# Optimization experiments

Measured on AMD Instinct MI355X. Metric: run time of the kernel, lower is better.

## Reference

```python
import jax, jax.numpy as jnp
import numpy as np

INPUT_DIM, LATENT_DIM, NUM_HEADS, LATENT_RANK = 2048, 1024, 16, 256
HEAD_DIM = LATENT_DIM // NUM_HEADS


def _linear_params(key, in_dim, out_dim):
    kw, kb = jax.random.split(key)
    bound = 1.0 / np.sqrt(in_dim)
    W = jax.random.uniform(kw, (in_dim, out_dim), jnp.float32, -bound, bound)
    b = jax.random.uniform(kb, (out_dim,), jnp.float32, -bound, bound)
    return W, b


def setup_inputs() -> dict:
    key = jax.random.key(0)
    ks = jax.random.split(key, 7)
    latent = jax.random.normal(ks[0], (2, 1024, LATENT_DIM), jnp.float32)
    x = jax.random.normal(ks[1], (2, 4096, INPUT_DIM), jnp.float32)
    Wq, bq = _linear_params(ks[2], LATENT_DIM, LATENT_DIM)
    Wc, bc = _linear_params(ks[3], INPUT_DIM, LATENT_RANK)
    Wk, bk = _linear_params(ks[4], LATENT_RANK, LATENT_DIM)
    Wv, bv = _linear_params(ks[5], LATENT_RANK, LATENT_DIM)
    Wo, bo = _linear_params(ks[6], LATENT_DIM, LATENT_DIM)
    return {"latent": latent, "x": x,
            "Wq": Wq, "bq": bq, "Wc": Wc, "bc": bc,
            "Wk": Wk, "bk": bk, "Wv": Wv, "bv": bv,
            "Wo": Wo, "bo": bo}


def reference(latent, x, Wq, bq, Wc, bc, Wk, bk, Wv, bv, Wo, bo):
    B, L, _ = latent.shape
    S = x.shape[1]
    H, D = NUM_HEADS, HEAD_DIM
    Q = (latent @ Wq + bq).reshape(B, L, H, D).transpose(0, 2, 1, 3)   # (B,H,L,D)
    compressed = x @ Wc + bc                                            # (B,S,R)
    K = (compressed @ Wk + bk).reshape(B, S, H, D).transpose(0, 2, 1, 3)  # (B,H,S,D)
    V = (compressed @ Wv + bv).reshape(B, S, H, D).transpose(0, 2, 1, 3)  # (B,H,S,D)
    scores = jnp.einsum('bhld,bhsd->bhls', Q, K) / np.sqrt(D).astype(jnp.float32)
    attn_weights = jax.nn.softmax(scores, axis=-1)                      # (B,H,L,S)
    attn_out = jnp.einsum('bhls,bhsd->bhld', attn_weights, V)           # (B,H,L,D)
    attn_out = attn_out.transpose(0, 2, 1, 3).reshape(B, L, H * D)
    output = attn_out @ Wo + bo                                         # (B,L,latent_dim)
    return output, attn_weights
```

## Files before the change

### kernel.cpp

```cpp
#include <hip/hip_runtime.h>

typedef short sv8 __attribute__((ext_vector_type(8)));
typedef float fv4 __attribute__((ext_vector_type(4)));

#define MFMA16(a, b, c) __builtin_amdgcn_mfma_f32_16x16x32_bf16((a), (b), (c), 0, 0, 0)

__device__ __forceinline__ unsigned short f2bf(float f) {
    unsigned u = __builtin_bit_cast(unsigned, f);
    unsigned r = (u + 0x7FFF + ((u >> 16) & 1)) >> 16;
    return (unsigned short)r;
}

constexpr int BB = 2, LL = 1024, SS = 4096, LD = 1024, HH = 16, DD = 64;

constexpr size_t NX = (size_t)2 * 4096 * 2048;
constexpr size_t NL = (size_t)2 * 1024 * 1024;

__global__ __launch_bounds__(256) void convert_inputs(
    const float* __restrict__ x, const float* __restrict__ latent,
    unsigned short* __restrict__ xb, unsigned short* __restrict__ lb)
{
    size_t i = ((size_t)blockIdx.x * 256 + threadIdx.x) * 8;
    const float* src; unsigned short* dst;
    if (i < NX) { src = x + i; dst = xb + i; }
    else        { size_t j = i - NX; src = latent + j; dst = lb + j; }
    float4 a = *(const float4*)src;
    float4 b = *(const float4*)(src + 4);
    ushort4 o0 = {f2bf(a.x), f2bf(a.y), f2bf(a.z), f2bf(a.w)};
    ushort4 o1 = {f2bf(b.x), f2bf(b.y), f2bf(b.z), f2bf(b.w)};
    *(ushort4*)dst = o0;
    *(ushort4*)(dst + 4) = o1;
}

__global__ __launch_bounds__(256) void transpose_weights(
    const float* __restrict__ Wc, const float* __restrict__ Wk, const float* __restrict__ Wv,
    const float* __restrict__ Wq, const float* __restrict__ Wo,
    unsigned short* __restrict__ Tc, unsigned short* __restrict__ Tk,
    unsigned short* __restrict__ Tv, unsigned short* __restrict__ Tq,
    unsigned short* __restrict__ To)
{
    __shared__ __align__(16) unsigned short tile[64][68];
    int bid = blockIdx.x;
    const float* W; unsigned short* T; int K, N, tix;
    if (bid < 128)      { W = Wc; T = Tc; K = 2048; N = 256;  tix = bid; }
    else if (bid < 192) { W = Wk; T = Tk; K = 256;  N = 1024; tix = bid - 128; }
    else if (bid < 256) { W = Wv; T = Tv; K = 256;  N = 1024; tix = bid - 192; }
    else if (bid < 512) { W = Wq; T = Tq; K = 1024; N = 1024; tix = bid - 256; }
    else                { W = Wo; T = To; K = 1024; N = 1024; tix = bid - 512; }
    int tn = N >> 6;
    int k0 = (tix / tn) << 6, n0 = (tix % tn) << 6;
    int t = threadIdx.x;
    int r = t >> 4, c4 = (t & 15) * 4;
#pragma unroll
    for (int i = 0; i < 4; i++) {
        int k = r + i * 16;
        float4 f = *(const float4*)(W + (size_t)(k0 + k) * N + n0 + c4);
        tile[k][c4 + 0] = f2bf(f.x); tile[k][c4 + 1] = f2bf(f.y);
        tile[k][c4 + 2] = f2bf(f.z); tile[k][c4 + 3] = f2bf(f.w);
    }
    __syncthreads();
#pragma unroll
    for (int i = 0; i < 4; i++) {
        int n = r + i * 16;
        ushort4 o;
        o.x = tile[c4 + 0][n]; o.y = tile[c4 + 1][n];
        o.z = tile[c4 + 2][n]; o.w = tile[c4 + 3][n];
        *(ushort4*)(T + (size_t)(n0 + n) * K + k0 + c4) = o;
    }
}

__global__ __launch_bounds__(256) void transpose_v(
    const unsigned short* __restrict__ V, unsigned short* __restrict__ Vt)
{
    __shared__ __align__(16) unsigned short tile[64][68];
    int s0 = blockIdx.x * 64;
    int h = blockIdx.y, b = blockIdx.z;
    int t = threadIdx.x;
    int r = t >> 4, c4 = (t & 15) * 4;
#pragma unroll
    for (int i = 0; i < 4; i++) {
        int s = r + i * 16;
        ushort4 v = *(const ushort4*)(V + (size_t)(b * SS + s0 + s) * LD + h * DD + c4);
        tile[s][c4 + 0] = v.x; tile[s][c4 + 1] = v.y;
        tile[s][c4 + 2] = v.z; tile[s][c4 + 3] = v.w;
    }
    __syncthreads();
#pragma unroll
    for (int i = 0; i < 4; i++) {
        int d = r + i * 16;
        ushort4 o;
        o.x = tile[c4 + 0][d]; o.y = tile[c4 + 1][d];
        o.z = tile[c4 + 2][d]; o.w = tile[c4 + 3][d];
        *(ushort4*)(Vt + ((size_t)(b * HH + h) * DD + d) * SS + s0 + c4) = o;
    }
}

template<int BM, int BN, bool C_F32>
__global__ __launch_bounds__(256) void gemm_bias(
    const unsigned short* __restrict__ Ag, const unsigned short* __restrict__ Bt,
    const float* __restrict__ bias, void* __restrict__ Cg,
    int M, int N, int K, float scale)
{
    constexpr int LDT = 40;
    __shared__ __align__(16) unsigned short As[BM * LDT];
    __shared__ __align__(16) unsigned short Bs[BN * LDT];
    __shared__ float bias_s[BN];
    const int t = threadIdx.x;
    const int m0 = blockIdx.x * BM, n0 = blockIdx.y * BN;
    for (int i = t; i < BN; i += 256) bias_s[i] = bias[n0 + i];
    const int w = t >> 6, lane = t & 63, l15 = lane & 15, quad = lane >> 4;
    constexpr int WM = BM / 2, WN = BN / 2;
    constexpr int MT = WM / 16, NT = WN / 16;
    const int wm = (w >> 1) * WM, wn = (w & 1) * WN;
    fv4 acc[MT][NT] = {};
    const int r4 = t >> 2, c8 = (t & 3) * 8;
    constexpr int AI = BM / 64, BI = BN / 64;
    const unsigned short* Aptr = Ag + (size_t)(m0 + r4) * K + c8;
    const unsigned short* Bptr = Bt + (size_t)(n0 + r4) * K + c8;
    sv8 areg[AI], breg[BI];
#pragma unroll
    for (int i = 0; i < AI; i++) areg[i] = *(const sv8*)(Aptr + (size_t)(i * 64) * K);
#pragma unroll
    for (int i = 0; i < BI; i++) breg[i] = *(const sv8*)(Bptr + (size_t)(i * 64) * K);
    for (int k0 = 0; k0 < K; k0 += 32) {
#pragma unroll
        for (int i = 0; i < AI; i++) *(sv8*)&As[(r4 + i * 64) * LDT + c8] = areg[i];
#pragma unroll
        for (int i = 0; i < BI; i++) *(sv8*)&Bs[(r4 + i * 64) * LDT + c8] = breg[i];
        __syncthreads();
        if (k0 + 32 < K) {
#pragma unroll
            for (int i = 0; i < AI; i++)
                areg[i] = *(const sv8*)(Aptr + (size_t)(i * 64) * K + k0 + 32);
#pragma unroll
            for (int i = 0; i < BI; i++)
                breg[i] = *(const sv8*)(Bptr + (size_t)(i * 64) * K + k0 + 32);
        }
        sv8 af[MT], bfr[NT];
#pragma unroll
        for (int mt = 0; mt < MT; mt++)
            af[mt] = *(const sv8*)&As[(wm + mt * 16 + l15) * LDT + quad * 8];
#pragma unroll
        for (int nt = 0; nt < NT; nt++)
            bfr[nt] = *(const sv8*)&Bs[(wn + nt * 16 + l15) * LDT + quad * 8];
#pragma unroll
        for (int mt = 0; mt < MT; mt++)
#pragma unroll
            for (int nt = 0; nt < NT; nt++)
                acc[mt][nt] = MFMA16(af[mt], bfr[nt], acc[mt][nt]);
        __syncthreads();
    }
#pragma unroll
    for (int mt = 0; mt < MT; mt++) {
#pragma unroll
        for (int nt = 0; nt < NT; nt++) {
            int col = n0 + wn + nt * 16 + l15;
            float bb = bias_s[wn + nt * 16 + l15];
#pragma unroll
            for (int r = 0; r < 4; r++) {
                int row = m0 + wm + mt * 16 + quad * 4 + r;
                float vv = (acc[mt][nt][r] + bb) * scale;
                if constexpr (C_F32) ((float*)Cg)[(size_t)row * N + col] = vv;
                else ((unsigned short*)Cg)[(size_t)row * N + col] = f2bf(vv);
            }
        }
    }
}

constexpr int SC  = 128;
constexpr int KLD = 72;
constexpr int VLD = 136;

__global__ __launch_bounds__(256) void attn_kernel(
    const unsigned short* __restrict__ Qw,
    const unsigned short* __restrict__ Kw,
    const unsigned short* __restrict__ Vtw,
    float* __restrict__ Wout,
    unsigned short* __restrict__ Ow)
{
    __shared__ __align__(16) unsigned short Ks[SC * KLD];
    __shared__ __align__(16) unsigned short Vs[DD * VLD];
    __shared__ __align__(16) unsigned short Ps[4 * 16 * VLD];
    const int bid = blockIdx.x;
    const int lt = bid & 15, h = (bid >> 4) & 15, b = bid >> 8;
    const int l0 = lt * 64;
    const int t = threadIdx.x, w = t >> 6, lane = t & 63, l15 = lane & 15, quad = lane >> 4;

    const unsigned short* qrow = Qw + (size_t)(b * LL + l0 + w * 16 + l15) * LD + h * DD;
    const sv8 aq0 = *(const sv8*)(qrow + quad * 8);
    const sv8 aq1 = *(const sv8*)(qrow + 32 + quad * 8);

    const unsigned short* kg0 = Kw + (size_t)(b * SS) * LD + h * DD;
    const int kr = t >> 3, kc = (t & 7) * 8;

    float lsum[4] = {0.f, 0.f, 0.f, 0.f};
    sv8 kreg[4];
#pragma unroll
    for (int i = 0; i < 4; i++)
        kreg[i] = *(const sv8*)(kg0 + (size_t)(kr + i * 32) * LD + kc);
    for (int s0 = 0; s0 < SS; s0 += SC) {
#pragma unroll
        for (int i = 0; i < 4; i++)
            *(sv8*)&Ks[(kr + i * 32) * KLD + kc] = kreg[i];
        __syncthreads();
        if (s0 + SC < SS) {
            const unsigned short* kg = kg0 + (size_t)(s0 + SC) * LD;
#pragma unroll
            for (int i = 0; i < 4; i++)
                kreg[i] = *(const sv8*)(kg + (size_t)(kr + i * 32) * LD + kc);
        }
#pragma unroll
        for (int c = 0; c < 8; c++) {
            sv8 b0 = *(const sv8*)&Ks[(c * 16 + l15) * KLD + quad * 8];
            sv8 b1 = *(const sv8*)&Ks[(c * 16 + l15) * KLD + 32 + quad * 8];
            fv4 sc = {0.f, 0.f, 0.f, 0.f};
            __builtin_amdgcn_s_setprio(1);
            sc = MFMA16(aq0, b0, sc);
            sc = MFMA16(aq1, b1, sc);
            __builtin_amdgcn_s_setprio(0);
#pragma unroll
            for (int r = 0; r < 4; r++) lsum[r] += __expf(sc[r]);
        }
        __syncthreads();
    }
    float inv_l[4];
#pragma unroll
    for (int r = 0; r < 4; r++) {
        float v = lsum[r];
        v += __shfl_xor(v, 1); v += __shfl_xor(v, 2);
        v += __shfl_xor(v, 4); v += __shfl_xor(v, 8);
        inv_l[r] = 1.0f / v;
    }

    fv4 oacc[4] = {};
    float* wbase = Wout + ((size_t)((b * HH + h) * LL + l0 + w * 16)) * SS;
    const unsigned short* vg0 = Vtw + (size_t)(b * HH + h) * DD * SS;
    const int vd = t >> 4, vc = (t & 15) * 8;
    sv8 vreg[4];
#pragma unroll
    for (int i = 0; i < 4; i++)
        kreg[i] = *(const sv8*)(kg0 + (size_t)(kr + i * 32) * LD + kc);
#pragma unroll
    for (int i = 0; i < 4; i++)
        vreg[i] = *(const sv8*)(vg0 + (size_t)(vd + i * 16) * SS + vc);
    for (int s0 = 0; s0 < SS; s0 += SC) {
#pragma unroll
        for (int i = 0; i < 4; i++)
            *(sv8*)&Ks[(kr + i * 32) * KLD + kc] = kreg[i];
#pragma unroll
        for (int i = 0; i < 4; i++)
            *(sv8*)&Vs[(vd + i * 16) * VLD + vc] = vreg[i];
        __syncthreads();
        if (s0 + SC < SS) {
            const unsigned short* kg = kg0 + (size_t)(s0 + SC) * LD;
#pragma unroll
            for (int i = 0; i < 4; i++)
                kreg[i] = *(const sv8*)(kg + (size_t)(kr + i * 32) * LD + kc);
#pragma unroll
            for (int i = 0; i < 4; i++)
                vreg[i] = *(const sv8*)(vg0 + (size_t)(vd + i * 16) * SS + s0 + SC + vc);
        }
        float* wp0 = wbase + s0;
#pragma unroll
        for (int c = 0; c < 8; c++) {
            sv8 b0 = *(const sv8*)&Ks[(c * 16 + l15) * KLD + quad * 8];
            sv8 b1 = *(const sv8*)&Ks[(c * 16 + l15) * KLD + 32 + quad * 8];
            fv4 sc = {0.f, 0.f, 0.f, 0.f};
            __builtin_amdgcn_s_setprio(1);
            sc = MFMA16(aq0, b0, sc);
            sc = MFMA16(aq1, b1, sc);
            __builtin_amdgcn_s_setprio(0);
#pragma unroll
            for (int r = 0; r < 4; r++) {
                float wv = __expf(sc[r]) * inv_l[r];
                wp0[(size_t)(quad * 4 + r) * SS + c * 16 + l15] = wv;
                Ps[(w * 16 + quad * 4 + r) * VLD + c * 16 + l15] = f2bf(wv);
            }
        }
        sv8 ap[4];
#pragma unroll
        for (int ks = 0; ks < 4; ks++)
            ap[ks] = *(const sv8*)&Ps[(w * 16 + l15) * VLD + ks * 32 + quad * 8];
        __builtin_amdgcn_s_setprio(1);
#pragma unroll
        for (int dt = 0; dt < 4; dt++)
#pragma unroll
            for (int ks = 0; ks < 4; ks++) {
                sv8 bv = *(const sv8*)&Vs[(dt * 16 + l15) * VLD + ks * 32 + quad * 8];
                oacc[dt] = MFMA16(ap[ks], bv, oacc[dt]);
            }
        __builtin_amdgcn_s_setprio(0);
        __syncthreads();
    }
    unsigned short* obase = Ow + (size_t)(b * LL + l0 + w * 16) * LD + h * DD;
#pragma unroll
    for (int dt = 0; dt < 4; dt++)
#pragma unroll
        for (int r = 0; r < 4; r++)
            obase[(size_t)(quad * 4 + r) * LD + dt * 16 + l15] = f2bf(oacc[dt][r]);
}

extern "C" void kernel_launch(void* const* d_in, const int* in_sizes, int n_in,
                              void* d_out, int out_size, void* d_ws, size_t ws_size,
                              hipStream_t stream) {
    const float* latent = (const float*)d_in[0];
    const float* x      = (const float*)d_in[1];
    const float* Wq = (const float*)d_in[2];
    const float* bq = (const float*)d_in[3];
    const float* Wc = (const float*)d_in[4];
    const float* bc = (const float*)d_in[5];
    const float* Wk = (const float*)d_in[6];
    const float* bk = (const float*)d_in[7];
    const float* Wv = (const float*)d_in[8];
    const float* bv = (const float*)d_in[9];
    const float* Wo = (const float*)d_in[10];
    const float* bo = (const float*)d_in[11];

    float* out   = (float*)d_out;
    float* attnw = out + (size_t)2 * 1024 * 1024;

    char* ws = (char*)d_ws;
    size_t off = 0;
    auto alloc = [&](size_t bytes) -> void* {
        void* p = ws + off; off += (bytes + 255) & ~(size_t)255; return p;
    };
    unsigned short* Tc   = (unsigned short*)alloc((size_t)2048 * 256 * 2);
    unsigned short* Tk   = (unsigned short*)alloc((size_t)1024 * 256 * 2);
    unsigned short* Tv   = (unsigned short*)alloc((size_t)1024 * 256 * 2);
    unsigned short* Tq   = (unsigned short*)alloc((size_t)1024 * 1024 * 2);
    unsigned short* To   = (unsigned short*)alloc((size_t)1024 * 1024 * 2);
    unsigned short* comp = (unsigned short*)alloc((size_t)8192 * 256 * 2);
    unsigned short* Kws  = (unsigned short*)alloc((size_t)8192 * 1024 * 2);
    unsigned short* Vws  = (unsigned short*)alloc((size_t)8192 * 1024 * 2);
    unsigned short* Vtws = (unsigned short*)alloc((size_t)8192 * 1024 * 2);
    unsigned short* Qws  = (unsigned short*)alloc((size_t)2048 * 1024 * 2);
    unsigned short* Ows  = (unsigned short*)alloc((size_t)2048 * 1024 * 2);

    unsigned short* xb = Kws;
    unsigned short* lb = Ows;

    convert_inputs<<<9216, 256, 0, stream>>>(x, latent, xb, lb);
    transpose_weights<<<768, 256, 0, stream>>>(Wc, Wk, Wv, Wq, Wo, Tc, Tk, Tv, Tq, To);
    gemm_bias<128, 64, false><<<dim3(64, 4), 256, 0, stream>>>(
        xb, Tc, bc, comp, 8192, 256, 2048, 1.0f);
    gemm_bias<64, 128, false><<<dim3(32, 8), 256, 0, stream>>>(
        lb, Tq, bq, Qws, 2048, 1024, 1024, 0.125f);
    gemm_bias<128, 128, false><<<dim3(64, 8), 256, 0, stream>>>(
        comp, Tk, bk, Kws, 8192, 1024, 256, 1.0f);
    gemm_bias<128, 128, false><<<dim3(64, 8), 256, 0, stream>>>(
        comp, Tv, bv, Vws, 8192, 1024, 256, 1.0f);
    transpose_v<<<dim3(64, 16, 2), 256, 0, stream>>>(Vws, Vtws);
    attn_kernel<<<512, 256, 0, stream>>>(Qws, Kws, Vtws, attnw, Ows);
    gemm_bias<64, 128, true><<<dim3(32, 8), 256, 0, stream>>>(
        Ows, To, bo, out, 2048, 1024, 1024, 1.0f);
}
```

Baseline: 842.8 us.

## Use direct global-to-LDS loads with double buffering and XOR swizzle in GEMM

The bias GEMM now loads A and B tiles straight from global memory into LDS with global_load_lds, dropping the register staging step. LDS is double-buffered, so the next K=64 tile streams in while the current one feeds MFMA, and there is one barrier per iteration instead of two. An XOR swizzle replaces the old row padding to avoid bank conflicts. The risks are higher LDS use per block, which can lower occupancy, and correctness relying on the barrier placement to order the asynchronous loads.

```diff
diff --git a/kernel.cpp b/kernel.cpp
--- a/kernel.cpp
+++ b/kernel.cpp
@@ -4,6 +4,13 @@
 typedef float fv4 __attribute__((ext_vector_type(4)));
 
 #define MFMA16(a, b, c) __builtin_amdgcn_mfma_f32_16x16x32_bf16((a), (b), (c), 0, 0, 0)
+
+__device__ __forceinline__ void gload16(const void* g, void* l) {
+    __builtin_amdgcn_global_load_lds(
+        (const __attribute__((address_space(1))) unsigned int*)(unsigned long long)g,
+        (__attribute__((address_space(3))) unsigned int*)(unsigned)(unsigned long long)l,
+        16, 0, 0);
+}
 
 __device__ __forceinline__ unsigned short f2bf(float f) {
     unsigned u = __builtin_bit_cast(unsigned, f);
@@ -101,65 +108,70 @@
     const float* __restrict__ bias, void* __restrict__ Cg,
     int M, int N, int K, float scale)
 {
-    constexpr int LDT = 40;
-    __shared__ __align__(16) unsigned short As[BM * LDT];
-    __shared__ __align__(16) unsigned short Bs[BN * LDT];
+    __shared__ __align__(16) unsigned short As[2][BM * 64];
+    __shared__ __align__(16) unsigned short Bs[2][BN * 64];
     __shared__ float bias_s[BN];
     const int t = threadIdx.x;
     const int m0 = blockIdx.x * BM, n0 = blockIdx.y * BN;
     for (int i = t; i < BN; i += 256) bias_s[i] = bias[n0 + i];
     const int w = t >> 6, lane = t & 63, l15 = lane & 15, quad = lane >> 4;
-    constexpr int WM = BM / 2, WN = BN / 2;
-    constexpr int MT = WM / 16, NT = WN / 16;
-    const int wm = (w >> 1) * WM, wn = (w & 1) * WN;
+    constexpr int MT = BM / 32, NT = BN / 32;
+    const int wm = (w >> 1) * (BM / 2), wn = (w & 1) * (BN / 2);
     fv4 acc[MT][NT] = {};
-    const int r4 = t >> 2, c8 = (t & 3) * 8;
-    constexpr int AI = BM / 64, BI = BN / 64;
-    const unsigned short* Aptr = Ag + (size_t)(m0 + r4) * K + c8;
-    const unsigned short* Bptr = Bt + (size_t)(n0 + r4) * K + c8;
-    sv8 areg[AI], breg[BI];
-#pragma unroll
-    for (int i = 0; i < AI; i++) areg[i] = *(const sv8*)(Aptr + (size_t)(i * 64) * K);
-#pragma unroll
-    for (int i = 0; i < BI; i++) breg[i] = *(const sv8*)(Bptr + (size_t)(i * 64) * K);
-    for (int k0 = 0; k0 < K; k0 += 32) {
-#pragma unroll
-        for (int i = 0; i < AI; i++) *(sv8*)&As[(r4 + i * 64) * LDT + c8] = areg[i];
-#pragma unroll
-        for (int i = 0; i < BI; i++) *(sv8*)&Bs[(r4 + i * 64) * LDT + c8] = breg[i];
-        __syncthreads();
-        if (k0 + 32 < K) {
-#pragma unroll
-            for (int i = 0; i < AI; i++)
-                areg[i] = *(const sv8*)(Aptr + (size_t)(i * 64) * K + k0 + 32);
-#pragma unroll
-            for (int i = 0; i < BI; i++)
-                breg[i] = *(const sv8*)(Bptr + (size_t)(i * 64) * K + k0 + 32);
-        }
-        sv8 af[MT], bfr[NT];
-#pragma unroll
-        for (int mt = 0; mt < MT; mt++)
-            af[mt] = *(const sv8*)&As[(wm + mt * 16 + l15) * LDT + quad * 8];
-#pragma unroll
-        for (int nt = 0; nt < NT; nt++)
-            bfr[nt] = *(const sv8*)&Bs[(wn + nt * 16 + l15) * LDT + quad * 8];
-#pragma unroll
-        for (int mt = 0; mt < MT; mt++)
+    const int srow = t >> 3;
+    const int usrc = ((t & 7) ^ (srow & 7)) << 3;
+    const unsigned short* ApG = Ag + (size_t)(m0 + srow) * K + usrc;
+    const unsigned short* BpG = Bt + (size_t)(n0 + srow) * K + usrc;
+    constexpr int PA = BM / 32, PB = BN / 32;
+    const int ldsw = w * 512;
+    const int ph0 = (quad ^ (l15 & 7)) << 3;
+
+    int bb = 0;
+#pragma unroll
+    for (int p = 0; p < PA; p++)
+        gload16(ApG + (size_t)(p * 32) * K, &As[0][p * 2048 + ldsw]);
+#pragma unroll
+    for (int p = 0; p < PB; p++)
+        gload16(BpG + (size_t)(p * 32) * K, &Bs[0][p * 2048 + ldsw]);
+    for (int k0 = 0; k0 < K; k0 += 64) {
+        __syncthreads();
+        if (k0 + 64 < K) {
+#pragma unroll
+            for (int p = 0; p < PA; p++)
+                gload16(ApG + (size_t)(p * 32) * K + k0 + 64, &As[bb ^ 1][p * 2048 + ldsw]);
+#pragma unroll
+            for (int p = 0; p < PB; p++)
+                gload16(BpG + (size_t)(p * 32) * K + k0 + 64, &Bs[bb ^ 1][p * 2048 + ldsw]);
+        }
+        sv8 af[2][MT], bf[2][NT];
+#pragma unroll
+        for (int h = 0; h < 2; h++) {
+#pragma unroll
+            for (int mt = 0; mt < MT; mt++)
+                af[h][mt] = *(const sv8*)&As[bb][(wm + mt * 16 + l15) * 64 + (ph0 ^ (h << 5))];
 #pragma unroll
             for (int nt = 0; nt < NT; nt++)
-                acc[mt][nt] = MFMA16(af[mt], bfr[nt], acc[mt][nt]);
-        __syncthreads();
+                bf[h][nt] = *(const sv8*)&Bs[bb][(wn + nt * 16 + l15) * 64 + (ph0 ^ (h << 5))];
+        }
+#pragma unroll
+        for (int h = 0; h < 2; h++)
+#pragma unroll
+            for (int mt = 0; mt < MT; mt++)
+#pragma unroll
+                for (int nt = 0; nt < NT; nt++)
+                    acc[mt][nt] = MFMA16(af[h][mt], bf[h][nt], acc[mt][nt]);
+        bb ^= 1;
     }
 #pragma unroll
     for (int mt = 0; mt < MT; mt++) {
 #pragma unroll
         for (int nt = 0; nt < NT; nt++) {
             int col = n0 + wn + nt * 16 + l15;
-            float bb = bias_s[wn + nt * 16 + l15];
+            float bb2 = bias_s[wn + nt * 16 + l15];
 #pragma unroll
             for (int r = 0; r < 4; r++) {
                 int row = m0 + wm + mt * 16 + quad * 4 + r;
-                float vv = (acc[mt][nt][r] + bb) * scale;
+                float vv = (acc[mt][nt][r] + bb2) * scale;
                 if constexpr (C_F32) ((float*)Cg)[(size_t)row * N + col] = vv;
                 else ((unsigned short*)Cg)[(size_t)row * N + col] = f2bf(vv);
             }
```

New measurement: 825.1 us. -2.1%, faster.
